# Optimization experiments

Measured on AMD Instinct MI355X. Metric: run time of the kernel, lower is better.

Reference implementation:

```python
import jax, jax.numpy as jnp
import numpy as np

TOP_K = 2


def setup_inputs() -> dict:
    key = jax.random.key(0)
    k1, k2, k3, k4, k5 = jax.random.split(key, 5)
    B, S, H, F, E = 2, 2048, 1024, 4096, 8
    scale = 0.02
    return {
        "hidden_states": jax.random.normal(k1, (B, S, H), dtype=jnp.float32),
        "w_gate": jax.random.normal(k2, (H, E), dtype=jnp.float32) * scale,
        "w_gate_proj": jax.random.normal(k3, (E, H, F), dtype=jnp.float32) * scale,
        "w_up_proj": jax.random.normal(k4, (E, H, F), dtype=jnp.float32) * scale,
        "w_down_proj": jax.random.normal(k5, (E, F, H), dtype=jnp.float32) * scale,
    }


def reference(hidden_states, w_gate, w_gate_proj, w_up_proj, w_down_proj):
    B, S, H = hidden_states.shape
    E = w_gate_proj.shape[0]
    x = hidden_states.reshape(-1, H)  # [T, H]

    # Router: softmax in float32, then top-k (NOT renormalized, matching source).
    router_logits = x @ w_gate  # [T, E]
    routing_probs = jax.nn.softmax(router_logits.astype(jnp.float32), axis=-1)
    routing_weights, selected_experts = jax.lax.top_k(routing_probs, TOP_K)  # [T, k]
    routing_weights = routing_weights.astype(x.dtype)

    out = jnp.zeros_like(x)
    # Small fixed loop over experts; per-token weight is zero for unrouted
    # tokens, so the masked dense computation is mathematically identical to
    # the gather/index_add dispatch in the source.
    for e in range(E):
        w_e = jnp.sum(routing_weights * (selected_experts == e), axis=-1)  # [T]
        h = jax.nn.silu(x @ w_gate_proj[e]) * (x @ w_up_proj[e])  # [T, F]
        out = out + (h @ w_down_proj[e]) * w_e[:, None]
    return out.reshape(B, S, H)
```

## Files before the change

kernel.cpp:

```cpp
#include <hip/hip_runtime.h>
#include <hip/hip_bf16.h>

#define T_TOK 4096
#define HDIM  1024
#define FDIM  4096
#define NEXP  8
#define CAP   4096
#define MAXWL 128
#define OBR   (2 * T_TOK + 128)

typedef __attribute__((ext_vector_type(8))) short short8;
typedef __attribute__((ext_vector_type(4))) float floatx4;
typedef __attribute__((ext_vector_type(4))) float float4v;
typedef __attribute__((ext_vector_type(4))) unsigned short ushort4v;

__device__ __forceinline__ unsigned short f2bf(float f) {
    union { float f; unsigned int u; } v; v.f = f;
    unsigned int u = v.u;
    u += 0x7fffu + ((u >> 16) & 1u);
    return (unsigned short)(u >> 16);
}

__device__ __forceinline__ void gl2lds16(const void* g, void* l) {
    __builtin_amdgcn_global_load_lds(
        (const __attribute__((address_space(1))) unsigned int*)g,
        (__attribute__((address_space(3))) unsigned int*)l,
        16, 0, 0);
}

__global__ void k_transpose_cast(const float* __restrict__ src, unsigned short* __restrict__ dst,
                                 int R, int C) {
    __shared__ float tile[64][65];
    size_t base = (size_t)blockIdx.z * (size_t)R * (size_t)C;
    int c0 = blockIdx.x * 64, r0 = blockIdx.y * 64;
    int lx = threadIdx.x & 15, ly = threadIdx.x >> 4;
#pragma unroll
    for (int i = 0; i < 4; ++i) {
        int rr = i * 16 + ly;
        float4v v = *(const float4v*)(src + base + (size_t)(r0 + rr) * C + c0 + lx * 4);
        tile[rr][lx * 4 + 0] = v[0]; tile[rr][lx * 4 + 1] = v[1];
        tile[rr][lx * 4 + 2] = v[2]; tile[rr][lx * 4 + 3] = v[3];
    }
    __syncthreads();
#pragma unroll
    for (int i = 0; i < 4; ++i) {
        int cc = i * 16 + ly;
        ushort4v o = { f2bf(tile[lx * 4 + 0][cc]), f2bf(tile[lx * 4 + 1][cc]),
                       f2bf(tile[lx * 4 + 2][cc]), f2bf(tile[lx * 4 + 3][cc]) };
        *(ushort4v*)(dst + base + (size_t)(c0 + cc) * R + r0 + lx * 4) = o;
    }
}

__global__ void k_router(const float* __restrict__ x, const float* __restrict__ wgate,
                         unsigned short* __restrict__ xb,
                         int* __restrict__ counts, int* __restrict__ ltok,
                         float* __restrict__ lwt, int* __restrict__ tslot) {
    int lane = threadIdx.x & 63;
    int tok = blockIdx.x * 4 + (threadIdx.x >> 6);
    const float* xr = x + (size_t)tok * HDIM;
    unsigned short* xbr = xb + (size_t)tok * HDIM;
    float acc[NEXP];
#pragma unroll
    for (int e = 0; e < NEXP; ++e) acc[e] = 0.f;
    for (int it = 0; it < HDIM / 256; ++it) {
        int h0 = it * 256 + lane * 4;
        float4v xv = *(const float4v*)(xr + h0);
        ushort4v xo = { f2bf(xv[0]), f2bf(xv[1]), f2bf(xv[2]), f2bf(xv[3]) };
        *(ushort4v*)(xbr + h0) = xo;
#pragma unroll
        for (int j = 0; j < 4; ++j) {
            float4v w0 = *(const float4v*)(wgate + (size_t)(h0 + j) * NEXP);
            float4v w1 = *(const float4v*)(wgate + (size_t)(h0 + j) * NEXP + 4);
            float xs = xv[j];
            acc[0] += xs * w0[0]; acc[1] += xs * w0[1];
            acc[2] += xs * w0[2]; acc[3] += xs * w0[3];
            acc[4] += xs * w1[0]; acc[5] += xs * w1[1];
            acc[6] += xs * w1[2]; acc[7] += xs * w1[3];
        }
    }
#pragma unroll
    for (int off = 32; off >= 1; off >>= 1)
#pragma unroll
        for (int e = 0; e < NEXP; ++e)
            acc[e] += __shfl_xor(acc[e], off, 64);
    if (lane == 0) {
        float m = acc[0];
#pragma unroll
        for (int e = 1; e < NEXP; ++e) m = fmaxf(m, acc[e]);
        float p[NEXP], s = 0.f;
#pragma unroll
        for (int e = 0; e < NEXP; ++e) { p[e] = __expf(acc[e] - m); s += p[e]; }
        float inv = 1.f / s;
#pragma unroll
        for (int e = 0; e < NEXP; ++e) p[e] *= inv;
        int e0 = 0; float b0 = p[0];
#pragma unroll
        for (int e = 1; e < NEXP; ++e) if (p[e] > b0) { b0 = p[e]; e0 = e; }
        int e1 = -1; float b1 = -1.f;
#pragma unroll
        for (int e = 0; e < NEXP; ++e) if (e != e0 && p[e] > b1) { b1 = p[e]; e1 = e; }
        int p0 = atomicAdd(&counts[e0], 1);
        ltok[e0 * CAP + p0] = tok; lwt[e0 * CAP + p0] = b0;
        int p1 = atomicAdd(&counts[e1], 1);
        ltok[e1 * CAP + p1] = tok; lwt[e1 * CAP + p1] = b1;
        tslot[tok * 2]     = (e0 << 16) | p0;
        tslot[tok * 2 + 1] = (e1 << 16) | p1;
    }
}

__global__ void k_prefix(const int* __restrict__ counts, int* __restrict__ offs,
                         int* __restrict__ wl, int* __restrict__ nwl) {
    if (threadIdx.x == 0) {
        int s = 0;
#pragma unroll
        for (int e = 0; e < NEXP; ++e) { offs[e] = s; s += counts[e]; }
        int n = 0;
        for (int e = 0; e < NEXP; ++e)
            for (int r = 0; r * 128 < counts[e] && n < MAXWL; ++r)
                wl[n++] = (e << 8) | r;
        nwl[0] = n;
    }
}

__global__ __launch_bounds__(256, 4)
void k_gemm1(const unsigned short* __restrict__ xb,
             const unsigned short* __restrict__ wgt,
             const unsigned short* __restrict__ wut,
             const int* __restrict__ counts, const int* __restrict__ offs,
             const int* __restrict__ ltok,
             const int* __restrict__ wl, const int* __restrict__ nwl,
             unsigned short* __restrict__ hbuf)
{
    if ((int)blockIdx.y >= nwl[0]) return;
    const int w = wl[blockIdx.y];
    const int e = w >> 8, rowtile = w & 255;
    const int M = counts[e];
    const int ftile = blockIdx.x;

    __shared__ __align__(16) unsigned short lA[2][128 * 32];
    __shared__ __align__(16) unsigned short lBg[2][64 * 32];
    __shared__ __align__(16) unsigned short lBu[2][64 * 32];
    __shared__ int stok[128];

    const int t = threadIdx.x;
    const int wave = t >> 6, lane = t & 63;

    if (t < 128) {
        int i = rowtile * 128 + t;
        stok[t] = (i < M) ? ltok[e * CAP + i] : ltok[e * CAP];
    }
    __syncthreads();

    const int r0 = t >> 2, k8 = t & 3;
    const int sw0 = (k8 ^ ((r0 >> 1) & 3)) * 8;
    const unsigned short* pA0 = xb + (size_t)stok[r0] * HDIM + sw0;
    const unsigned short* pA1 = xb + (size_t)stok[r0 + 64] * HDIM + sw0;
    const size_t wbase = (size_t)e * FDIM * HDIM + (size_t)(ftile * 64) * HDIM;
    const unsigned short* pG0 = wgt + wbase + (size_t)r0 * HDIM + sw0;
    const unsigned short* pU0 = wut + wbase + (size_t)r0 * HDIM + sw0;

    const int wm = wave >> 1, wn = wave & 1;
    const int fr = lane & 15, kg = lane >> 4;
    const int cswz = (kg ^ ((fr >> 1) & 3)) * 8;

    floatx4 accg[4][2], accu[4][2];
#pragma unroll
    for (int mi = 0; mi < 4; ++mi)
#pragma unroll
        for (int ni = 0; ni < 2; ++ni) {
            floatx4 z = {0.f, 0.f, 0.f, 0.f};
            accg[mi][ni] = z; accu[mi][ni] = z;
        }

    auto stage = [&](int b) {
        gl2lds16(pA0, &lA[b][wave * 512]);        pA0 += 32;
        gl2lds16(pA1, &lA[b][2048 + wave * 512]); pA1 += 32;
        gl2lds16(pG0, &lBg[b][wave * 512]);       pG0 += 32;
        gl2lds16(pU0, &lBu[b][wave * 512]);       pU0 += 32;
    };
    auto compute = [&](int b) {
        short8 a[4], g[2], u[2];
#pragma unroll
        for (int mi = 0; mi < 4; ++mi)
            a[mi] = *(const short8*)&lA[b][(wm * 64 + mi * 16 + fr) * 32 + cswz];
#pragma unroll
        for (int ni = 0; ni < 2; ++ni) {
            g[ni] = *(const short8*)&lBg[b][(wn * 32 + ni * 16 + fr) * 32 + cswz];
            u[ni] = *(const short8*)&lBu[b][(wn * 32 + ni * 16 + fr) * 32 + cswz];
        }
#pragma unroll
        for (int mi = 0; mi < 4; ++mi)
#pragma unroll
            for (int ni = 0; ni < 2; ++ni) {
                accg[mi][ni] = __builtin_amdgcn_mfma_f32_16x16x32_bf16(a[mi], g[ni], accg[mi][ni], 0, 0, 0);
                accu[mi][ni] = __builtin_amdgcn_mfma_f32_16x16x32_bf16(a[mi], u[ni], accu[mi][ni], 0, 0, 0);
            }
    };

    stage(0);
    __syncthreads();
#pragma unroll 1
    for (int it = 0; it < 16; ++it) {
        stage(1);
        compute(0);
        __syncthreads();
        if (it < 15) stage(0);
        compute(1);
        __syncthreads();
    }

    const int hrow0 = offs[e] + rowtile * 128;
#pragma unroll
    for (int mi = 0; mi < 4; ++mi)
#pragma unroll
        for (int ni = 0; ni < 2; ++ni) {
            int c = ftile * 64 + wn * 32 + ni * 16 + fr;
#pragma unroll
            for (int r = 0; r < 4; ++r) {
                int rr = wm * 64 + mi * 16 + kg * 4 + r;
                if (rowtile * 128 + rr < M) {
                    float g = accg[mi][ni][r];
                    float val = (g / (1.f + __expf(-g))) * accu[mi][ni][r];
                    hbuf[(size_t)(hrow0 + rr) * FDIM + c] = f2bf(val);
                }
            }
        }
}

__global__ __launch_bounds__(256, 2)
void k_gemm2(const unsigned short* __restrict__ hbuf,
             const unsigned short* __restrict__ wdt,
             const int* __restrict__ counts, const int* __restrict__ offs,
             const float* __restrict__ lwt,
             const int* __restrict__ wl, const int* __restrict__ nwl,
             float* __restrict__ obuf)
{
    if ((int)blockIdx.y >= nwl[0]) return;
    const int w = wl[blockIdx.y];
    const int e = w >> 8, rowtile = w & 255;
    const int M = counts[e];
    const int htile = blockIdx.x;
    const int khalf = blockIdx.z;

    __shared__ __align__(16) unsigned short lA[2][128 * 32];
    __shared__ __align__(16) unsigned short lB[2][128 * 32];
    __shared__ float swt[128];

    const int t = threadIdx.x;
    const int wave = t >> 6, lane = t & 63;

    if (t < 128) {
        int i = rowtile * 128 + t;
        swt[t] = (i < M) ? lwt[e * CAP + i] : 0.f;
    }

    const int row0 = offs[e] + rowtile * 128;
    const int r0 = t >> 2, k8 = t & 3;
    const int kofs = khalf * (FDIM / 2);
    const int sw0 = (k8 ^ ((r0 >> 1) & 3)) * 8;
    const unsigned short* pA0 = hbuf + (size_t)(row0 + r0) * FDIM + kofs + sw0;
    const unsigned short* pA1 = hbuf + (size_t)(row0 + 64 + r0) * FDIM + kofs + sw0;
    const size_t wb = (size_t)e * HDIM * FDIM + (size_t)(htile * 128) * FDIM;
    const unsigned short* pB0 = wdt + wb + (size_t)r0 * FDIM + kofs + sw0;
    const unsigned short* pB1 = wdt + wb + (size_t)(64 + r0) * FDIM + kofs + sw0;

    const int wm = wave >> 1, wn = wave & 1;
    const int fr = lane & 15, kg = lane >> 4;
    const int cswz = (kg ^ ((fr >> 1) & 3)) * 8;

    floatx4 acc[4][4];
#pragma unroll
    for (int mi = 0; mi < 4; ++mi)
#pragma unroll
        for (int ni = 0; ni < 4; ++ni) {
            floatx4 z = {0.f, 0.f, 0.f, 0.f};
            acc[mi][ni] = z;
        }

    auto stage = [&](int b) {
        gl2lds16(pA0, &lA[b][wave * 512]);        pA0 += 32;
        gl2lds16(pA1, &lA[b][2048 + wave * 512]); pA1 += 32;
        gl2lds16(pB0, &lB[b][wave * 512]);        pB0 += 32;
        gl2lds16(pB1, &lB[b][2048 + wave * 512]); pB1 += 32;
    };
    auto compute = [&](int b) {
        short8 a[4], bb[4];
#pragma unroll
        for (int mi = 0; mi < 4; ++mi)
            a[mi] = *(const short8*)&lA[b][(wm * 64 + mi * 16 + fr) * 32 + cswz];
#pragma unroll
        for (int ni = 0; ni < 4; ++ni)
            bb[ni] = *(const short8*)&lB[b][(wn * 64 + ni * 16 + fr) * 32 + cswz];
#pragma unroll
        for (int mi = 0; mi < 4; ++mi)
#pragma unroll
            for (int ni = 0; ni < 4; ++ni)
                acc[mi][ni] = __builtin_amdgcn_mfma_f32_16x16x32_bf16(a[mi], bb[ni], acc[mi][ni], 0, 0, 0);
    };

    stage(0);
    __syncthreads();
#pragma unroll 1
    for (int it = 0; it < 32; ++it) {
        stage(1);
        compute(0);
        __syncthreads();
        if (it < 31) stage(0);
        compute(1);
        __syncthreads();
    }

    float* ob = obuf + (size_t)khalf * OBR * HDIM;
#pragma unroll
    for (int mi = 0; mi < 4; ++mi)
#pragma unroll
        for (int ni = 0; ni < 4; ++ni) {
            int c = htile * 128 + wn * 64 + ni * 16 + fr;
#pragma unroll
            for (int r = 0; r < 4; ++r) {
                int rr = wm * 64 + mi * 16 + kg * 4 + r;
                if (rowtile * 128 + rr < M)
                    ob[(size_t)(row0 + rr) * HDIM + c] = acc[mi][ni][r] * swt[rr];
            }
        }
}

__global__ void k_combine(const float* __restrict__ obuf, const int* __restrict__ tslot,
                          const int* __restrict__ offs, float* __restrict__ out) {
    int gid = blockIdx.x * 256 + threadIdx.x;
    int tok = gid >> 8;
    int c = (gid & 255) * 4;
    int s0 = tslot[tok * 2], s1 = tslot[tok * 2 + 1];
    size_t r0 = (size_t)(offs[s0 >> 16] + (s0 & 0xFFFF));
    size_t r1 = (size_t)(offs[s1 >> 16] + (s1 & 0xFFFF));
    float4v v00 = *(const float4v*)(obuf + r0 * HDIM + c);
    float4v v01 = *(const float4v*)(obuf + ((size_t)OBR + r0) * HDIM + c);
    float4v v10 = *(const float4v*)(obuf + r1 * HDIM + c);
    float4v v11 = *(const float4v*)(obuf + ((size_t)OBR + r1) * HDIM + c);
    float4v s = v00 + v01 + v10 + v11;
    *(float4v*)(out + (size_t)tok * HDIM + c) = s;
}

extern "C" void kernel_launch(void* const* d_in, const int* in_sizes, int n_in,
                              void* d_out, int out_size, void* d_ws, size_t ws_size,
                              hipStream_t stream) {
    const float* x     = (const float*)d_in[0];
    const float* wgate = (const float*)d_in[1];
    const float* wg    = (const float*)d_in[2];
    const float* wu    = (const float*)d_in[3];
    const float* wd    = (const float*)d_in[4];
    float* out = (float*)d_out;

    char* ws = (char*)d_ws;
    size_t off = 0;
    unsigned short* xb  = (unsigned short*)(ws + off); off += (size_t)T_TOK * HDIM * 2;
    unsigned short* wgt = (unsigned short*)(ws + off); off += (size_t)NEXP * FDIM * HDIM * 2;
    unsigned short* wut = (unsigned short*)(ws + off); off += (size_t)NEXP * FDIM * HDIM * 2;
    unsigned short* wdt = (unsigned short*)(ws + off); off += (size_t)NEXP * HDIM * FDIM * 2;
    unsigned short* hbuf= (unsigned short*)(ws + off); off += (size_t)OBR * FDIM * 2;
    int*   ltok   = (int*)(ws + off);   off += (size_t)NEXP * CAP * 4;
    float* lwt    = (float*)(ws + off); off += (size_t)NEXP * CAP * 4;
    int*   tslot  = (int*)(ws + off);   off += (size_t)T_TOK * 2 * 4;
    int*   counts = (int*)(ws + off);   off += 256;
    int*   offs   = (int*)(ws + off);   off += 256;
    int*   wl     = (int*)(ws + off);   off += MAXWL * 4;
    int*   nwl    = (int*)(ws + off);   off += 256;
    float* obuf = (float*)wgt;

    hipMemsetAsync(counts, 0, 32, stream);

    k_router<<<T_TOK / 4, 256, 0, stream>>>(x, wgate, xb, counts, ltok, lwt, tslot);
    k_transpose_cast<<<dim3(FDIM / 64, HDIM / 64, NEXP), 256, 0, stream>>>(wg, wgt, HDIM, FDIM);
    k_transpose_cast<<<dim3(FDIM / 64, HDIM / 64, NEXP), 256, 0, stream>>>(wu, wut, HDIM, FDIM);
    k_transpose_cast<<<dim3(HDIM / 64, FDIM / 64, NEXP), 256, 0, stream>>>(wd, wdt, FDIM, HDIM);
    k_prefix<<<1, 64, 0, stream>>>(counts, offs, wl, nwl);
    k_gemm1<<<dim3(FDIM / 64, 72), 256, 0, stream>>>(xb, wgt, wut, counts, offs, ltok, wl, nwl, hbuf);
    k_gemm2<<<dim3(HDIM / 128, 72, 2), 256, 0, stream>>>(hbuf, wdt, counts, offs, lwt, wl, nwl, obuf);
    k_combine<<<T_TOK * HDIM / 1024, 256, 0, stream>>>(obuf, tslot, offs, out);
}
```

Before: 834.2 us.

## Remap GEMM block indices for XCD-aware weight reuse and merge gate/up transposes

Both expert GEMMs now use a flattened 1D grid whose block-index decode places blocks of the same row tile in a fixed order. In gemm1 each F-tile is pinned to one XCD via bid&7, so a given weight tile is reused from that die's L2. The gate and up weight transpose-casts are merged into one launch, and gemm2's launch bound is raised to 4 blocks per SM for more occupancy. The higher occupancy hint may force register spills in gemm2.

```diff
diff --git a/kernel.cpp b/kernel.cpp
--- a/kernel.cpp
+++ b/kernel.cpp
@@ -32,6 +32,33 @@
                                  int R, int C) {
     __shared__ float tile[64][65];
     size_t base = (size_t)blockIdx.z * (size_t)R * (size_t)C;
+    int c0 = blockIdx.x * 64, r0 = blockIdx.y * 64;
+    int lx = threadIdx.x & 15, ly = threadIdx.x >> 4;
+#pragma unroll
+    for (int i = 0; i < 4; ++i) {
+        int rr = i * 16 + ly;
+        float4v v = *(const float4v*)(src + base + (size_t)(r0 + rr) * C + c0 + lx * 4);
+        tile[rr][lx * 4 + 0] = v[0]; tile[rr][lx * 4 + 1] = v[1];
+        tile[rr][lx * 4 + 2] = v[2]; tile[rr][lx * 4 + 3] = v[3];
+    }
+    __syncthreads();
+#pragma unroll
+    for (int i = 0; i < 4; ++i) {
+        int cc = i * 16 + ly;
+        ushort4v o = { f2bf(tile[lx * 4 + 0][cc]), f2bf(tile[lx * 4 + 1][cc]),
+                       f2bf(tile[lx * 4 + 2][cc]), f2bf(tile[lx * 4 + 3][cc]) };
+        *(ushort4v*)(dst + base + (size_t)(c0 + cc) * R + r0 + lx * 4) = o;
+    }
+}
+
+__global__ void k_transpose_cast2(const float* __restrict__ s0, const float* __restrict__ s1,
+                                  unsigned short* __restrict__ d0, unsigned short* __restrict__ d1) {
+    const int R = HDIM, C = FDIM;
+    __shared__ float tile[64][65];
+    int m = blockIdx.z >> 3, zz = blockIdx.z & 7;
+    const float* src = (m ? s1 : s0);
+    unsigned short* dst = (m ? d1 : d0);
+    size_t base = (size_t)zz * (size_t)R * (size_t)C;
     int c0 = blockIdx.x * 64, r0 = blockIdx.y * 64;
     int lx = threadIdx.x & 15, ly = threadIdx.x >> 4;
 #pragma unroll
@@ -131,11 +158,16 @@
              const int* __restrict__ wl, const int* __restrict__ nwl,
              unsigned short* __restrict__ hbuf)
 {
-    if ((int)blockIdx.y >= nwl[0]) return;
-    const int w = wl[blockIdx.y];
+    const int bid = blockIdx.x;
+    const int xcd = bid & 7;
+    const int jj  = bid >> 3;
+    const int fhi = jj & 7;
+    const int by  = jj >> 3;
+    if (by >= nwl[0]) return;
+    const int ftile = xcd + 8 * fhi;
+    const int w = wl[by];
     const int e = w >> 8, rowtile = w & 255;
     const int M = counts[e];
-    const int ftile = blockIdx.x;
 
     __shared__ __align__(16) unsigned short lA[2][128 * 32];
     __shared__ __align__(16) unsigned short lBg[2][64 * 32];
@@ -227,7 +259,7 @@
         }
 }
 
-__global__ __launch_bounds__(256, 2)
+__global__ __launch_bounds__(256, 4)
 void k_gemm2(const unsigned short* __restrict__ hbuf,
              const unsigned short* __restrict__ wdt,
              const int* __restrict__ counts, const int* __restrict__ offs,
@@ -235,12 +267,15 @@
              const int* __restrict__ wl, const int* __restrict__ nwl,
              float* __restrict__ obuf)
 {
-    if ((int)blockIdx.y >= nwl[0]) return;
-    const int w = wl[blockIdx.y];
+    const int bid = blockIdx.x;
+    const int htile = bid & 7;
+    const int jj = bid >> 3;
+    const int khalf = jj & 1;
+    const int by = jj >> 1;
+    if (by >= nwl[0]) return;
+    const int w = wl[by];
     const int e = w >> 8, rowtile = w & 255;
     const int M = counts[e];
-    const int htile = blockIdx.x;
-    const int khalf = blockIdx.z;
 
     __shared__ __align__(16) unsigned short lA[2][128 * 32];
     __shared__ __align__(16) unsigned short lB[2][128 * 32];
@@ -370,11 +405,10 @@
     hipMemsetAsync(counts, 0, 32, stream);
 
     k_router<<<T_TOK / 4, 256, 0, stream>>>(x, wgate, xb, counts, ltok, lwt, tslot);
-    k_transpose_cast<<<dim3(FDIM / 64, HDIM / 64, NEXP), 256, 0, stream>>>(wg, wgt, HDIM, FDIM);
-    k_transpose_cast<<<dim3(FDIM / 64, HDIM / 64, NEXP), 256, 0, stream>>>(wu, wut, HDIM, FDIM);
+    k_transpose_cast2<<<dim3(FDIM / 64, HDIM / 64, 16), 256, 0, stream>>>(wg, wu, wgt, wut);
     k_transpose_cast<<<dim3(HDIM / 64, FDIM / 64, NEXP), 256, 0, stream>>>(wd, wdt, FDIM, HDIM);
     k_prefix<<<1, 64, 0, stream>>>(counts, offs, wl, nwl);
-    k_gemm1<<<dim3(FDIM / 64, 72), 256, 0, stream>>>(xb, wgt, wut, counts, offs, ltok, wl, nwl, hbuf);
-    k_gemm2<<<dim3(HDIM / 128, 72, 2), 256, 0, stream>>>(hbuf, wdt, counts, offs, lwt, wl, nwl, obuf);
+    k_gemm1<<<8 * 8 * 72, 256, 0, stream>>>(xb, wgt, wut, counts, offs, ltok, wl, nwl, hbuf);
+    k_gemm2<<<8 * 2 * 72, 256, 0, stream>>>(hbuf, wdt, counts, offs, lwt, wl, nwl, obuf);
     k_combine<<<T_TOK * HDIM / 1024, 256, 0, stream>>>(obuf, tslot, offs, out);
 }
```

After: 827.5 us. No clear change (-0.8%).
